# Optimization experiments

Measured on AMD Instinct MI355X. Metric: run time of the kernel, lower is better.

## Reference

```python
import jax, jax.numpy as jnp
import numpy as np

B, K, H, W = 16, 32, 28, 28   # batch, set size, image h, image w
HID, OUT = 64, 64             # hid_dim, out_dim
NOPS = 8                      # permutation-equivariant 3->3 pool/broadcast basis ops


def setup_inputs() -> dict:
    key = jax.random.key(0)
    ks = jax.random.split(key, 8)
    def p(k, shape, fan_in):
        return jax.random.normal(k, shape, jnp.float32) / np.float32(np.sqrt(fan_in))
    return dict(
        x=jax.random.normal(ks[0], (B, K, H, W), jnp.float32),
        conv1_w=p(ks[1], (32, 1, 3, 3), 9),
        conv1_b=jnp.zeros((32,), jnp.float32),
        conv2_w=p(ks[2], (64, 32, 3, 3), 32 * 9),
        conv2_b=jnp.zeros((64,), jnp.float32),
        fc_w=p(ks[3], (HID, 64 * 7 * 7), 64 * 7 * 7),
        fc_b=jnp.zeros((HID,), jnp.float32),
        eq_w=p(ks[4], (HID, OUT, NOPS), HID * NOPS),
        eq_b=jnp.zeros((OUT,), jnp.float32),
        out_w=p(ks[5], (1, OUT), OUT),
        out_b=jnp.zeros((1,), jnp.float32),
    )


def _conv2d(x, w, b):
    y = jax.lax.conv_general_dilated(x, w, (1, 1), 'SAME',
                                     dimension_numbers=('NCHW', 'OIHW', 'NCHW'))
    return y + b[None, :, None, None]


def _maxpool2(x):
    return jax.lax.reduce_window(x, -jnp.inf, jax.lax.max,
                                 (1, 1, 2, 2), (1, 1, 2, 2), 'VALID')


def _forward(x, conv1_w, conv1_b, conv2_w, conv2_b, fc_w, fc_b, eq_w, eq_b, out_w, out_b):
    # --- BasicConvNet embed: (B*K, 1, H, W) -> (B*K, HID) ---
    x1 = x.reshape(B * K, 1, H, W)
    h1 = _maxpool2(jax.nn.relu(_conv2d(x1, conv1_w, conv1_b)))   # (B*K, 32, 14, 14)
    h2 = _maxpool2(jax.nn.relu(_conv2d(h1, conv2_w, conv2_b)))   # (B*K, 64, 7, 7)
    feat = jax.nn.relu(h2.reshape(B * K, -1) @ fc_w.T + fc_b)    # (B*K, HID)
    x4 = feat.reshape(B, K, HID)

    # --- triple outer product: (B, HID, K, K, K), no contracted index ---
    x5 = jnp.einsum('bid,bjd,bkd->bdijk', x4, x4, x4)

    # --- SetEq3to3: 8 equivariant pool/broadcast basis ops, contracted with eq_w[d,e,o].
    # Contract each pooled tensor with its slice of eq_w BEFORE broadcasting (same math,
    # avoids materializing 8 full (B,d,K,K,K) op tensors). ---
    m_i  = x5.mean(2)           # (B, d, j, k)
    m_j  = x5.mean(3)           # (B, d, i, k)
    m_k  = x5.mean(4)           # (B, d, i, j)
    m_ij = m_i.mean(2)          # (B, d, k)
    m_ik = m_i.mean(3)          # (B, d, j)
    m_jk = m_j.mean(3)          # (B, d, i)
    m_all = m_ij.mean(2)        # (B, d)

    x6 = (jnp.einsum('bdijk,de->beijk', x5, eq_w[:, :, 0])
          + jnp.einsum('bdjk,de->bejk', m_i, eq_w[:, :, 1])[:, :, None, :, :]
          + jnp.einsum('bdik,de->beik', m_j, eq_w[:, :, 2])[:, :, :, None, :]
          + jnp.einsum('bdij,de->beij', m_k, eq_w[:, :, 3])[:, :, :, :, None]
          + jnp.einsum('bdk,de->bek', m_ij, eq_w[:, :, 4])[:, :, None, None, :]
          + jnp.einsum('bdj,de->bej', m_ik, eq_w[:, :, 5])[:, :, None, :, None]
          + jnp.einsum('bdi,de->bei', m_jk, eq_w[:, :, 6])[:, :, :, None, None]
          + jnp.einsum('bd,de->be', m_all, eq_w[:, :, 7])[:, :, None, None, None]
          + eq_b[None, :, None, None, None])          # (B, OUT, K, K, K)

    # permute to channels-last, relu, pool over (i,j,k), relu, final linear
    x7 = jax.nn.relu(x6.transpose(0, 2, 3, 4, 1))     # (B, K, K, K, OUT)
    x8 = x7.mean(axis=(1, 2, 3))                      # (B, OUT)
    x9 = jax.nn.relu(x8)
    # dropout_prob = 0 -> identity
    return x9 @ out_w.T + out_b                       # (B, 1)


def reference(x, conv1_w, conv1_b, conv2_w, conv2_b, fc_w, fc_b, eq_w, eq_b, out_w, out_b):
    return _forward(x, conv1_w, conv1_b, conv2_w, conv2_b, fc_w, fc_b,
                    eq_w, eq_b, out_w, out_b)
```

## Files before the change

kernel.cpp:

```cpp
#include <hip/hip_runtime.h>
#include <hip/hip_bf16.h>


typedef __attribute__((ext_vector_type(8))) short short8;
typedef __attribute__((ext_vector_type(4))) float f32x4;

__device__ __forceinline__ f32x4 mfma_bf16(short8 a, short8 b, f32x4 c) {
  return __builtin_amdgcn_mfma_f32_16x16x32_bf16(a, b, c, 0, 0, 0);
}

__device__ __forceinline__ unsigned short f2bs(float f) {
  unsigned int u = __float_as_uint(f);
  unsigned int r = u + 0x7fffu + ((u >> 16) & 1u);
  return (unsigned short)(r >> 16);
}
__device__ __forceinline__ unsigned int pk2(float x, float y) {
  union { __hip_bfloat162 h; unsigned int u; } cv;
  cv.h = __float22bfloat162_rn(make_float2(x, y));
  return cv.u;
}
__device__ __forceinline__ void ub8(const short* p, float* f) {
  uint4 u = *(const uint4*)p;
  f[0] = __uint_as_float(u.x << 16); f[1] = __uint_as_float(u.x & 0xffff0000u);
  f[2] = __uint_as_float(u.y << 16); f[3] = __uint_as_float(u.y & 0xffff0000u);
  f[4] = __uint_as_float(u.z << 16); f[5] = __uint_as_float(u.z & 0xffff0000u);
  f[6] = __uint_as_float(u.w << 16); f[7] = __uint_as_float(u.w & 0xffff0000u);
}

__global__ __launch_bounds__(256, 2) void k12_conv(const float* __restrict__ x,
    const float* __restrict__ w1, const float* __restrict__ b1,
    const float* __restrict__ w2, const float* __restrict__ b2,
    short* __restrict__ h2b,
    const float* __restrict__ eqw, float* __restrict__ W7t, short* __restrict__ Wtb,
    const float* __restrict__ fcw, short* __restrict__ fcwb) {
  const int n = blockIdx.x, t = threadIdx.x;
  if (n >= 512) {
    if (n < 520) {
      const int m = n - 512;
      for (int idx = t; idx < 4096; idx += 256) {
        int e = idx >> 6, d = idx & 63;
        float v = eqw[d*512 + e*8 + m];
        if (m == 7) W7t[idx] = v;
        else        Wtb[m*4096 + idx] = (short)f2bs(v);
      }
    } else {
      int base = (n - 520)*12544 + t;
      for (int q = 0; q < 49; ++q) {
        int idx = base + q*256;
        fcwb[idx] = (short)f2bs(fcw[idx]);
      }
    }
    return;
  }
  __shared__ float si[30*30];
  __shared__ float sw[32*9];
  __shared__ float sb[32];
  __shared__ __align__(16) short inT[16*18*40];
  const int wv = t >> 6, l = t & 63, quad = l >> 4, col = l & 15;

  const int c_out = wv*16 + col;
  float w72[72];
  {
    const float4* src = (const float4*)(w2 + c_out*288 + quad*72);
#pragma unroll
    for (int q = 0; q < 18; ++q) {
      float4 v = src[q];
      w72[q*4+0] = v.x; w72[q*4+1] = v.y; w72[q*4+2] = v.z; w72[q*4+3] = v.w;
    }
  }
  union SU { short8 v; unsigned int u[4]; };
  short8 Bq[9];
#pragma unroll
  for (int dd = 0; dd < 9; ++dd) {
    SU b;
#pragma unroll
    for (int q = 0; q < 4; ++q)
      b.u[q] = pk2(w72[(2*q)*9 + dd], w72[(2*q+1)*9 + dd]);
    Bq[dd] = b.v;
  }
  const float bb2 = b2[c_out];

  for (int idx = t; idx < 900; idx += 256) si[idx] = 0.f;
  {
    unsigned int* zp = (unsigned int*)inT;
    for (int idx = t; idx < 5760; idx += 256) zp[idx] = 0u;
  }
  for (int idx = t; idx < 288; idx += 256) sw[idx] = w1[idx];
  if (t < 32) sb[t] = b1[t];
  __syncthreads();
  for (int idx = t; idx < 784; idx += 256) {
    int y = idx / 28, xx = idx - y*28;
    si[(y+1)*30 + xx + 1] = x[n*784 + idx];
  }
  __syncthreads();

  {
    const int cg = t & 7;
    float wreg[4][9], breg[4];
#pragma unroll
    for (int cc = 0; cc < 4; ++cc) {
      breg[cc] = sb[cg*4 + cc];
#pragma unroll
      for (int q = 0; q < 9; ++q) wreg[cc][q] = sw[(cg*4 + cc)*9 + q];
    }
    for (int idx = t; idx < 1568; idx += 256) {
      int pos = idx >> 3;
      int py = pos / 14, px = pos - py*14;
      float pt[4][4];
#pragma unroll
      for (int r = 0; r < 4; ++r)
#pragma unroll
        for (int q = 0; q < 4; ++q)
          pt[r][q] = si[(2*py + r)*30 + 2*px + q];
      float res[4];
#pragma unroll
      for (int cc = 0; cc < 4; ++cc) {
        float best = 0.f;
#pragma unroll
        for (int a = 0; a < 2; ++a)
#pragma unroll
          for (int b3 = 0; b3 < 2; ++b3) {
            float v = breg[cc]
              + wreg[cc][0]*pt[a+0][b3+0] + wreg[cc][1]*pt[a+0][b3+1] + wreg[cc][2]*pt[a+0][b3+2]
              + wreg[cc][3]*pt[a+1][b3+0] + wreg[cc][4]*pt[a+1][b3+1] + wreg[cc][5]*pt[a+1][b3+2]
              + wreg[cc][6]*pt[a+2][b3+0] + wreg[cc][7]*pt[a+2][b3+1] + wreg[cc][8]*pt[a+2][b3+2];
            best = fmaxf(best, v);
          }
        res[cc] = best;
      }
      uint2 pkd;
      pkd.x = pk2(res[0], res[1]);
      pkd.y = pk2(res[2], res[3]);
      *(uint2*)&inT[(py+1)*720 + (px+1)*40 + cg*4] = pkd;
    }
  }
  __syncthreads();

  for (int p = 0; p < 7; ++p) {
    short8 Ar[4][3];
#pragma unroll
    for (int rr = 0; rr < 4; ++rr)
#pragma unroll
      for (int dx = 0; dx < 3; ++dx)
        Ar[rr][dx] = *(const short8*)&inT[(2*p + rr)*720 + (col + dx)*40 + quad*8];
    f32x4 a0 = {0.f,0.f,0.f,0.f}, a1 = {0.f,0.f,0.f,0.f};
#pragma unroll
    for (int dy = 0; dy < 3; ++dy)
#pragma unroll
      for (int dx = 0; dx < 3; ++dx) {
        a0 = mfma_bf16(Ar[dy][dx],     Bq[dy*3 + dx], a0);
        a1 = mfma_bf16(Ar[dy + 1][dx], Bq[dy*3 + dx], a1);
      }
#pragma unroll
    for (int a = 0; a < 2; ++a) {
      int px = quad*2 + a;
      if (px < 7) {
        float m0 = fmaxf(fmaxf(a0[2*a], a0[2*a + 1]), fmaxf(a1[2*a], a1[2*a + 1]));
        h2b[n*3136 + c_out*49 + p*7 + px] = (short)f2bs(fmaxf(m0 + bb2, 0.f));
      }
    }
  }
}

__global__ __launch_bounds__(256) void k3_mfma(const short* __restrict__ h2b,
    const short* __restrict__ fcwb, float* __restrict__ part) {
  const int blk = blockIdx.x, kp = blockIdx.y, t = threadIdx.x;
  const int w = t >> 6, l = t & 63, quad = l >> 4, col = l & 15;
  const int mt = w & 1, nh = w >> 1;
  const int img = blk*32 + mt*16 + col;
  const short* Ap = h2b + img*3136 + kp*224 + quad*8;
  const short* B0 = fcwb + (nh*32 + col)*3136 + kp*224 + quad*8;
  const short* B1 = fcwb + (nh*32 + 16 + col)*3136 + kp*224 + quad*8;
  f32x4 acc0 = {0.f,0.f,0.f,0.f}, acc1 = {0.f,0.f,0.f,0.f};
#pragma unroll
  for (int q = 0; q < 7; ++q) {
    short8 A  = *(const short8*)(Ap + q*32);
    short8 b0 = *(const short8*)(B0 + q*32);
    short8 b1 = *(const short8*)(B1 + q*32);
    acc0 = mfma_bf16(A, b0, acc0);
    acc1 = mfma_bf16(A, b1, acc1);
  }
  const int e0 = nh*32 + col, e1 = e0 + 16;
  const int base = blk*32 + mt*16 + quad*4;
  float* dst = part + kp*32768;
#pragma unroll
  for (int r = 0; r < 4; ++r) {
    dst[(base + r)*64 + e0] = acc0[r];
    dst[(base + r)*64 + e1] = acc1[r];
  }
}

__global__ __launch_bounds__(256) void k4_prep(const float* __restrict__ part,
    const float* __restrict__ fb, const float* __restrict__ W7t,
    const float* __restrict__ eqb, float* __restrict__ feat,
    float* __restrict__ s, float* __restrict__ t7c) {
  __shared__ __align__(16) float sf[2048];
  __shared__ float ss[64];
  const int b = blockIdx.x, t = threadIdx.x;
  for (int v4 = t; v4 < 512; v4 += 256) {
    float4 a = {0.f, 0.f, 0.f, 0.f};
#pragma unroll
    for (int kp = 0; kp < 14; ++kp) {
      float4 p = *(const float4*)&part[kp*32768 + b*2048 + v4*4];
      a.x += p.x; a.y += p.y; a.z += p.z; a.w += p.w;
    }
    float4 fbv = *(const float4*)&fb[(v4*4) & 63];
    float4 r;
    r.x = fmaxf(a.x + fbv.x, 0.f);
    r.y = fmaxf(a.y + fbv.y, 0.f);
    r.z = fmaxf(a.z + fbv.z, 0.f);
    r.w = fmaxf(a.w + fbv.w, 0.f);
    *(float4*)&sf[v4*4] = r;
    *(float4*)&feat[b*2048 + v4*4] = r;
  }
  __syncthreads();
  if (t < 64) {
    float a = 0.f;
    for (int i = 0; i < 32; ++i) a += sf[i*64 + t];
    a *= (1.f/32.f);
    s[b*64 + t] = a;
    ss[t] = a;
  }
  __syncthreads();
  if (t < 64) {
    const float* W7 = W7t + t*64;
    float t7 = 0.f;
    for (int d = 0; d < 64; ++d) {
      float sv = ss[d];
      t7 += sv*sv*sv * W7[d];
    }
    t7c[b*64 + t] = t7 + eqb[t];
  }
}

__global__ __launch_bounds__(256, 2) void k5_mfma(const float* __restrict__ feat,
    const float* __restrict__ s_, const short* __restrict__ Wtb,
    const float* __restrict__ t7c, float* __restrict__ x8p) {
  __shared__ __align__(16) float Fm[32*68];
  __shared__ __align__(16) float FI[64];
  __shared__ __align__(16) float SV[64];
  __shared__ __align__(16) float C0[64];
  __shared__ float C0P[128];
  __shared__ float KCf[32*68];
  __shared__ float JCf[32*68];
  __shared__ float RED[256];
  __shared__ __align__(16) short Fb[32*72];
  __shared__ __align__(16) short QPb[64*72];
  __shared__ __align__(16) short G2b[64*72];
  __shared__ __align__(16) short G3b[64*72];

  const int i = blockIdx.x, b = blockIdx.y, t = threadIdx.x;
  const int w = t >> 6, l = t & 63, quad = l >> 4, col = l & 15;

  for (int idx = t; idx < 2048; idx += 256) {
    int r = idx >> 6, d = idx & 63;
    float v = feat[b*2048 + idx];
    Fm[r*68 + d] = v;
    Fb[r*72 + d] = (short)f2bs(v);
  }
  if (t < 64) { FI[t] = feat[b*2048 + i*64 + t]; SV[t] = s_[b*64 + t]; }
  __syncthreads();

  {
    const int e = t >> 2, dbase = (t & 3) * 16;
#pragma unroll
    for (int h = 0; h < 2; ++h) {
      int off = dbase + h*8;
      float w0[8], w1[8], w2[8], w3[8], w4[8], w5[8];
      ub8(&Wtb[0*4096 + e*64 + off], w0);
      ub8(&Wtb[1*4096 + e*64 + off], w1);
      ub8(&Wtb[2*4096 + e*64 + off], w2);
      ub8(&Wtb[3*4096 + e*64 + off], w3);
      ub8(&Wtb[4*4096 + e*64 + off], w4);
      ub8(&Wtb[5*4096 + e*64 + off], w5);
      uint4 qv, g2v, g3v;
      unsigned int* qp = &qv.x;
      unsigned int* g2p = &g2v.x;
      unsigned int* g3p = &g3v.x;
#pragma unroll
      for (int j = 0; j < 4; ++j) {
        float fi0 = FI[off + 2*j],     fi1 = FI[off + 2*j + 1];
        float s0  = SV[off + 2*j],     s1  = SV[off + 2*j + 1];
        float q0 = fi0*w0[2*j]   + s0*w1[2*j];
        float q1 = fi1*w0[2*j+1] + s1*w1[2*j+1];
        float a0 = s0*(fi0*w2[2*j]   + s0*w4[2*j]);
        float a1 = s1*(fi1*w2[2*j+1] + s1*w4[2*j+1]);
        float c0 = s0*(fi0*w3[2*j]   + s0*w5[2*j]);
        float c1 = s1*(fi1*w3[2*j+1] + s1*w5[2*j+1]);
        qp[j]  = pk2(q0, q1);
        g2p[j] = pk2(a0, a1);
        g3p[j] = pk2(c0, c1);
      }
      *(uint4*)&QPb[e*72 + off] = qv;
      *(uint4*)&G2b[e*72 + off] = g2v;
      *(uint4*)&G3b[e*72 + off] = g3v;
    }
  }
  if (t < 128) {
    int e = t & 63, dh = t >> 6;
    const short* W6 = Wtb + 6*4096 + e*64 + dh*32;
    float a = 0.f;
#pragma unroll
    for (int g = 0; g < 4; ++g) {
      float wf[8];
      ub8(&W6[g*8], wf);
#pragma unroll
      for (int dd = 0; dd < 8; ++dd) {
        int d = dh*32 + g*8 + dd;
        float sd = SV[d];
        a += sd*sd*FI[d]*wf[dd];
      }
    }
    C0P[dh*64 + e] = a;
  }
  __syncthreads();

  if (w < 2) {
    const short* G = w ? G3b : G2b;
    float* DST = w ? JCf : KCf;
    short8 Bf[4][2];
#pragma unroll
    for (int n = 0; n < 4; ++n)
#pragma unroll
      for (int s2 = 0; s2 < 2; ++s2)
        Bf[n][s2] = *(const short8*)&G[(n*16 + col)*72 + s2*32 + quad*8];
#pragma unroll
    for (int m = 0; m < 2; ++m) {
      short8 A0 = *(const short8*)&Fb[(m*16 + col)*72 + quad*8];
      short8 A1 = *(const short8*)&Fb[(m*16 + col)*72 + 32 + quad*8];
#pragma unroll
      for (int n = 0; n < 4; ++n) {
        f32x4 z = {0.f, 0.f, 0.f, 0.f};
        f32x4 ac = mfma_bf16(A1, Bf[n][1], mfma_bf16(A0, Bf[n][0], z));
#pragma unroll
        for (int r = 0; r < 4; ++r)
          DST[(m*16 + quad*4 + r)*68 + n*16 + col] = ac[r];
      }
    }
  } else if (w == 2) {
    C0[l] = C0P[l] + C0P[64 + l] + t7c[b*64 + l];
  }
  __syncthreads();

  float c0v[4];
#pragma unroll
  for (int n = 0; n < 4; ++n) c0v[n] = C0[n*16 + col];
  float jcq[8][4];
#pragma unroll
  for (int jj = 0; jj < 8; ++jj)
#pragma unroll
    for (int n = 0; n < 4; ++n)
      jcq[jj][n] = JCf[(w*8 + jj)*68 + n*16 + col] + c0v[n];
  float kcv[2][4][4];
#pragma unroll
  for (int kb2 = 0; kb2 < 2; ++kb2)
#pragma unroll
    for (int r = 0; r < 4; ++r)
#pragma unroll
      for (int n = 0; n < 4; ++n)
        kcv[kb2][r][n] = KCf[(kb2*16 + quad*4 + r)*68 + n*16 + col];
  short8 Bq[4][2];
#pragma unroll
  for (int n = 0; n < 4; ++n)
#pragma unroll
    for (int s2 = 0; s2 < 2; ++s2)
      Bq[n][s2] = *(const short8*)&QPb[(n*16 + col)*72 + s2*32 + quad*8];

  float4 fkv[2][4];
#pragma unroll
  for (int kb2 = 0; kb2 < 2; ++kb2) {
    const float* fk = &Fm[(kb2*16 + col)*68 + quad*8];
    fkv[kb2][0] = *(const float4*)(fk);
    fkv[kb2][1] = *(const float4*)(fk + 4);
    fkv[kb2][2] = *(const float4*)(fk + 32);
    fkv[kb2][3] = *(const float4*)(fk + 36);
  }

  float sum[4] = {0.f, 0.f, 0.f, 0.f};
  union SU { short8 v; unsigned int u[4]; };

#pragma unroll
  for (int jj = 0; jj < 8; ++jj) {
    const float* fj = &Fm[(w*8 + jj)*68 + quad*8];
    float4 j0 = *(const float4*)(fj);
    float4 j1 = *(const float4*)(fj + 4);
    float4 j2 = *(const float4*)(fj + 32);
    float4 j3 = *(const float4*)(fj + 36);
#pragma unroll
    for (int kb2 = 0; kb2 < 2; ++kb2) {
      float4 k0 = fkv[kb2][0], k1 = fkv[kb2][1];
      float4 k2v = fkv[kb2][2], k3v = fkv[kb2][3];
      SU A0, A1;
      A0.u[0] = pk2(j0.x*k0.x, j0.y*k0.y);
      A0.u[1] = pk2(j0.z*k0.z, j0.w*k0.w);
      A0.u[2] = pk2(j1.x*k1.x, j1.y*k1.y);
      A0.u[3] = pk2(j1.z*k1.z, j1.w*k1.w);
      A1.u[0] = pk2(j2.x*k2v.x, j2.y*k2v.y);
      A1.u[1] = pk2(j2.z*k2v.z, j2.w*k2v.w);
      A1.u[2] = pk2(j3.x*k3v.x, j3.y*k3v.y);
      A1.u[3] = pk2(j3.z*k3v.z, j3.w*k3v.w);
      f32x4 ac[4];
#pragma unroll
      for (int n = 0; n < 4; ++n) {
        f32x4 z = {0.f, 0.f, 0.f, 0.f};
        ac[n] = mfma_bf16(A1.v, Bq[n][1], mfma_bf16(A0.v, Bq[n][0], z));
      }
#pragma unroll
      for (int n = 0; n < 4; ++n)
#pragma unroll
        for (int r = 0; r < 4; ++r) {
          float v = ac[n][r] + kcv[kb2][r][n] + jcq[jj][n];
          sum[n] += fmaxf(v, 0.f);
        }
    }
  }

#pragma unroll
  for (int n = 0; n < 4; ++n) {
    float v = sum[n];
    v += __shfl_xor(v, 16, 64);
    v += __shfl_xor(v, 32, 64);
    if (l < 16) RED[w*64 + n*16 + l] = v;
  }
  __syncthreads();
  if (t < 64) {
    float tot = RED[t] + RED[64 + t] + RED[128 + t] + RED[192 + t];
    x8p[(b*32 + i)*64 + t] = tot;
  }
}

__global__ __launch_bounds__(64) void k6_out(const float* __restrict__ x8p,
    const float* __restrict__ ow, const float* __restrict__ ob,
    float* __restrict__ out) {
  const int bb = blockIdx.x, t = threadIdx.x;
  float a = 0.f;
#pragma unroll
  for (int i = 0; i < 32; ++i) a += x8p[(bb*32 + i)*64 + t];
  float v = fmaxf(a * (1.f/32768.f), 0.f) * ow[t];
#pragma unroll
  for (int off = 32; off > 0; off >>= 1) v += __shfl_down(v, off, 64);
  if (t == 0) out[bb] = v + ob[0];
}

extern "C" void kernel_launch(void* const* d_in, const int* in_sizes, int n_in,
                              void* d_out, int out_size, void* d_ws, size_t ws_size,
                              hipStream_t stream) {
  const float* x   = (const float*)d_in[0];
  const float* c1w = (const float*)d_in[1];
  const float* c1b = (const float*)d_in[2];
  const float* c2w = (const float*)d_in[3];
  const float* c2b = (const float*)d_in[4];
  const float* fcw = (const float*)d_in[5];
  const float* fcb = (const float*)d_in[6];
  const float* eqw = (const float*)d_in[7];
  const float* eqb = (const float*)d_in[8];
  const float* ow  = (const float*)d_in[9];
  const float* ob  = (const float*)d_in[10];
  float* out = (float*)d_out;

  short* h2b  = (short*)d_ws;
  float* feat = (float*)(h2b + 512*3136);
  float* s    = feat + 32768;
  float* t7c  = s + 1024;
  float* x8p  = t7c + 1024;
  float* W7t  = x8p + 32768;
  short* Wtb  = (short*)(W7t + 4096);
  short* fcwb = Wtb + 7*4096;
  float* part = (float*)(fcwb + 200704);

  hipLaunchKernelGGL(k12_conv, dim3(536), dim3(256), 0, stream,
                     x, c1w, c1b, c2w, c2b, h2b, eqw, W7t, Wtb, fcw, fcwb);
  hipLaunchKernelGGL(k3_mfma,  dim3(16, 14), dim3(256), 0, stream, h2b, fcwb, part);
  hipLaunchKernelGGL(k4_prep,  dim3(16),  dim3(256), 0, stream,
                     part, fcb, W7t, eqb, feat, s, t7c);
  hipLaunchKernelGGL(k5_mfma,  dim3(32, 16), dim3(256), 0, stream, feat, s, Wtb, t7c, x8p);
  hipLaunchKernelGGL(k6_out,   dim3(16),  dim3(64),  0, stream, x8p, ow, ob, out);
}
```

Measured before the change: 122.9 us.

## Fuse FC layer into conv kernel and move set-mean prep into equivariant kernel

Weight conversion moves into a separate small prep kernel, which also pre-packs conv2 weights into bf16 MFMA fragment order so each conv block loads them directly. The conv kernel now keeps pooled conv2 output in shared memory and computes the FC layer per image with a scalar dot product, removing the bf16 h2 round-trip, the split-K partial buffer, and the k3/k4 launches. The set mean and cubic term are recomputed inside each equivariant block. In exchange, every conv block streams the full bf16 FC weight matrix, the FC uses scalar FMAs instead of MFMA, the shared-memory footprint grows, and the prep kernel now runs serially before the conv.

```diff
diff --git a/kernel.cpp b/kernel.cpp
--- a/kernel.cpp
+++ b/kernel.cpp
@@ -27,56 +27,53 @@
   f[6] = __uint_as_float(u.w << 16); f[7] = __uint_as_float(u.w & 0xffff0000u);
 }
 
-__global__ __launch_bounds__(256, 2) void k12_conv(const float* __restrict__ x,
+__global__ __launch_bounds__(256) void k0_prep(const float* __restrict__ eqw,
+    const float* __restrict__ w2, const float* __restrict__ fcw,
+    float* __restrict__ W7t, short* __restrict__ Wtb,
+    short* __restrict__ w2p, short* __restrict__ fcwb) {
+  const int b = blockIdx.x, t = threadIdx.x;
+  if (b < 8) {
+    const int m = b;
+    for (int idx = t; idx < 4096; idx += 256) {
+      int e = idx >> 6, d = idx & 63;
+      float v = eqw[d*512 + e*8 + m];
+      if (m == 7) W7t[idx] = v;
+      else        Wtb[m*4096 + idx] = (short)f2bs(v);
+    }
+  } else if (b == 8) {
+    for (int idx = t; idx < 18432; idx += 256) {
+      int s2 = idx & 7, c = (idx >> 3) & 63, quad = (idx >> 9) & 3, dd = idx >> 11;
+      w2p[idx] = (short)f2bs(w2[c*288 + (quad*8 + s2)*9 + dd]);
+    }
+  } else {
+    int base = (b - 9)*12544 + t;
+    for (int q = 0; q < 49; ++q) {
+      int idx = base + q*256;
+      fcwb[idx] = (short)f2bs(fcw[idx]);
+    }
+  }
+}
+
+__global__ __launch_bounds__(256, 2) void kA_conv(const float* __restrict__ x,
     const float* __restrict__ w1, const float* __restrict__ b1,
-    const float* __restrict__ w2, const float* __restrict__ b2,
-    short* __restrict__ h2b,
-    const float* __restrict__ eqw, float* __restrict__ W7t, short* __restrict__ Wtb,
-    const float* __restrict__ fcw, short* __restrict__ fcwb) {
+    const short* __restrict__ w2p, const float* __restrict__ b2,
+    const short* __restrict__ fcwb, const float* __restrict__ fcb,
+    float* __restrict__ feat) {
   const int n = blockIdx.x, t = threadIdx.x;
-  if (n >= 512) {
-    if (n < 520) {
-      const int m = n - 512;
-      for (int idx = t; idx < 4096; idx += 256) {
-        int e = idx >> 6, d = idx & 63;
-        float v = eqw[d*512 + e*8 + m];
-        if (m == 7) W7t[idx] = v;
-        else        Wtb[m*4096 + idx] = (short)f2bs(v);
-      }
-    } else {
-      int base = (n - 520)*12544 + t;
-      for (int q = 0; q < 49; ++q) {
-        int idx = base + q*256;
-        fcwb[idx] = (short)f2bs(fcw[idx]);
-      }
-    }
-    return;
-  }
   __shared__ float si[30*30];
   __shared__ float sw[32*9];
   __shared__ float sb[32];
   __shared__ __align__(16) short inT[16*18*40];
+  __shared__ __align__(16) float h2f[3136];
+  __shared__ float sf4[256];
   const int wv = t >> 6, l = t & 63, quad = l >> 4, col = l & 15;
 
   const int c_out = wv*16 + col;
-  float w72[72];
+  short8 Bq[9];
   {
-    const float4* src = (const float4*)(w2 + c_out*288 + quad*72);
-#pragma unroll
-    for (int q = 0; q < 18; ++q) {
-      float4 v = src[q];
-      w72[q*4+0] = v.x; w72[q*4+1] = v.y; w72[q*4+2] = v.z; w72[q*4+3] = v.w;
-    }
-  }
-  union SU { short8 v; unsigned int u[4]; };
-  short8 Bq[9];
-#pragma unroll
-  for (int dd = 0; dd < 9; ++dd) {
-    SU b;
-#pragma unroll
-    for (int q = 0; q < 4; ++q)
-      b.u[q] = pk2(w72[(2*q)*9 + dd], w72[(2*q+1)*9 + dd]);
-    Bq[dd] = b.v;
+    const short8* wp = (const short8*)w2p + quad*64 + c_out;
+#pragma unroll
+    for (int dd = 0; dd < 9; ++dd) Bq[dd] = wp[dd*256];
   }
   const float bb2 = b2[c_out];
 
@@ -156,89 +153,41 @@
       int px = quad*2 + a;
       if (px < 7) {
         float m0 = fmaxf(fmaxf(a0[2*a], a0[2*a + 1]), fmaxf(a1[2*a], a1[2*a + 1]));
-        h2b[n*3136 + c_out*49 + p*7 + px] = (short)f2bs(fmaxf(m0 + bb2, 0.f));
-      }
-    }
-  }
-}
-
-__global__ __launch_bounds__(256) void k3_mfma(const short* __restrict__ h2b,
-    const short* __restrict__ fcwb, float* __restrict__ part) {
-  const int blk = blockIdx.x, kp = blockIdx.y, t = threadIdx.x;
-  const int w = t >> 6, l = t & 63, quad = l >> 4, col = l & 15;
-  const int mt = w & 1, nh = w >> 1;
-  const int img = blk*32 + mt*16 + col;
-  const short* Ap = h2b + img*3136 + kp*224 + quad*8;
-  const short* B0 = fcwb + (nh*32 + col)*3136 + kp*224 + quad*8;
-  const short* B1 = fcwb + (nh*32 + 16 + col)*3136 + kp*224 + quad*8;
-  f32x4 acc0 = {0.f,0.f,0.f,0.f}, acc1 = {0.f,0.f,0.f,0.f};
-#pragma unroll
-  for (int q = 0; q < 7; ++q) {
-    short8 A  = *(const short8*)(Ap + q*32);
-    short8 b0 = *(const short8*)(B0 + q*32);
-    short8 b1 = *(const short8*)(B1 + q*32);
-    acc0 = mfma_bf16(A, b0, acc0);
-    acc1 = mfma_bf16(A, b1, acc1);
-  }
-  const int e0 = nh*32 + col, e1 = e0 + 16;
-  const int base = blk*32 + mt*16 + quad*4;
-  float* dst = part + kp*32768;
-#pragma unroll
-  for (int r = 0; r < 4; ++r) {
-    dst[(base + r)*64 + e0] = acc0[r];
-    dst[(base + r)*64 + e1] = acc1[r];
-  }
-}
-
-__global__ __launch_bounds__(256) void k4_prep(const float* __restrict__ part,
-    const float* __restrict__ fb, const float* __restrict__ W7t,
-    const float* __restrict__ eqb, float* __restrict__ feat,
-    float* __restrict__ s, float* __restrict__ t7c) {
-  __shared__ __align__(16) float sf[2048];
-  __shared__ float ss[64];
-  const int b = blockIdx.x, t = threadIdx.x;
-  for (int v4 = t; v4 < 512; v4 += 256) {
-    float4 a = {0.f, 0.f, 0.f, 0.f};
-#pragma unroll
-    for (int kp = 0; kp < 14; ++kp) {
-      float4 p = *(const float4*)&part[kp*32768 + b*2048 + v4*4];
-      a.x += p.x; a.y += p.y; a.z += p.z; a.w += p.w;
-    }
-    float4 fbv = *(const float4*)&fb[(v4*4) & 63];
-    float4 r;
-    r.x = fmaxf(a.x + fbv.x, 0.f);
-    r.y = fmaxf(a.y + fbv.y, 0.f);
-    r.z = fmaxf(a.z + fbv.z, 0.f);
-    r.w = fmaxf(a.w + fbv.w, 0.f);
-    *(float4*)&sf[v4*4] = r;
-    *(float4*)&feat[b*2048 + v4*4] = r;
+        h2f[c_out*49 + p*7 + px] = fmaxf(m0 + bb2, 0.f);
+      }
+    }
+  }
+  {
+    const short* Wrow = fcwb + l*3136 + wv*784;
+    const float* Hrow = h2f + wv*784;
+    float a0 = 0.f, a1 = 0.f, a2 = 0.f, a3 = 0.f;
+#pragma unroll 7
+    for (int j = 0; j < 98; ++j) {
+      float wf[8]; ub8(&Wrow[j*8], wf);
+      float4 hx = *(const float4*)&Hrow[j*8];
+      float4 hy = *(const float4*)&Hrow[j*8 + 4];
+      a0 += wf[0]*hx.x + wf[4]*hy.x;
+      a1 += wf[1]*hx.y + wf[5]*hy.y;
+      a2 += wf[2]*hx.z + wf[6]*hy.z;
+      a3 += wf[3]*hx.w + wf[7]*hy.w;
+    }
+    sf4[wv*64 + l] = (a0 + a1) + (a2 + a3);
   }
   __syncthreads();
   if (t < 64) {
-    float a = 0.f;
-    for (int i = 0; i < 32; ++i) a += sf[i*64 + t];
-    a *= (1.f/32.f);
-    s[b*64 + t] = a;
-    ss[t] = a;
-  }
-  __syncthreads();
-  if (t < 64) {
-    const float* W7 = W7t + t*64;
-    float t7 = 0.f;
-    for (int d = 0; d < 64; ++d) {
-      float sv = ss[d];
-      t7 += sv*sv*sv * W7[d];
-    }
-    t7c[b*64 + t] = t7 + eqb[t];
+    float v = sf4[t] + sf4[64 + t] + sf4[128 + t] + sf4[192 + t] + fcb[t];
+    feat[n*64 + t] = fmaxf(v, 0.f);
   }
 }
 
 __global__ __launch_bounds__(256, 2) void k5_mfma(const float* __restrict__ feat,
-    const float* __restrict__ s_, const short* __restrict__ Wtb,
-    const float* __restrict__ t7c, float* __restrict__ x8p) {
+    const short* __restrict__ Wtb, const float* __restrict__ W7t,
+    const float* __restrict__ eqb, float* __restrict__ x8p) {
   __shared__ __align__(16) float Fm[32*68];
   __shared__ __align__(16) float FI[64];
   __shared__ __align__(16) float SV[64];
+  __shared__ __align__(16) float SC[64];
+  __shared__ __align__(16) float TC[64];
   __shared__ __align__(16) float C0[64];
   __shared__ float C0P[128];
   __shared__ float KCf[32*68];
@@ -258,21 +207,42 @@
     Fm[r*68 + d] = v;
     Fb[r*72 + d] = (short)f2bs(v);
   }
-  if (t < 64) { FI[t] = feat[b*2048 + i*64 + t]; SV[t] = s_[b*64 + t]; }
-  __syncthreads();
+  if (t < 64) FI[t] = feat[b*2048 + i*64 + t];
+  __syncthreads();
+
+  if (t < 64) {
+    float a = 0.f;
+#pragma unroll
+    for (int r = 0; r < 32; ++r) a += Fm[r*68 + t];
+    a *= (1.f/32.f);
+    SV[t] = a;
+    SC[t] = a*a*a;
+  }
+  __syncthreads();
+
+  if (t < 64) {
+    const float* W7 = W7t + t*64;
+    float acc = 0.f;
+#pragma unroll
+    for (int d = 0; d < 64; d += 4) {
+      float4 w4 = *(const float4*)&W7[d];
+      acc += SC[d]*w4.x + SC[d+1]*w4.y + SC[d+2]*w4.z + SC[d+3]*w4.w;
+    }
+    TC[t] = acc + eqb[t];
+  }
 
   {
     const int e = t >> 2, dbase = (t & 3) * 16;
 #pragma unroll
     for (int h = 0; h < 2; ++h) {
       int off = dbase + h*8;
-      float w0[8], w1[8], w2[8], w3[8], w4[8], w5[8];
+      float w0[8], w1r[8], w2r[8], w3r[8], w4r[8], w5r[8];
       ub8(&Wtb[0*4096 + e*64 + off], w0);
-      ub8(&Wtb[1*4096 + e*64 + off], w1);
-      ub8(&Wtb[2*4096 + e*64 + off], w2);
-      ub8(&Wtb[3*4096 + e*64 + off], w3);
-      ub8(&Wtb[4*4096 + e*64 + off], w4);
-      ub8(&Wtb[5*4096 + e*64 + off], w5);
+      ub8(&Wtb[1*4096 + e*64 + off], w1r);
+      ub8(&Wtb[2*4096 + e*64 + off], w2r);
+      ub8(&Wtb[3*4096 + e*64 + off], w3r);
+      ub8(&Wtb[4*4096 + e*64 + off], w4r);
+      ub8(&Wtb[5*4096 + e*64 + off], w5r);
       uint4 qv, g2v, g3v;
       unsigned int* qp = &qv.x;
       unsigned int* g2p = &g2v.x;
@@ -281,12 +251,12 @@
       for (int j = 0; j < 4; ++j) {
         float fi0 = FI[off + 2*j],     fi1 = FI[off + 2*j + 1];
         float s0  = SV[off + 2*j],     s1  = SV[off + 2*j + 1];
-        float q0 = fi0*w0[2*j]   + s0*w1[2*j];
-        float q1 = fi1*w0[2*j+1] + s1*w1[2*j+1];
-        float a0 = s0*(fi0*w2[2*j]   + s0*w4[2*j]);
-        float a1 = s1*(fi1*w2[2*j+1] + s1*w4[2*j+1]);
-        float c0 = s0*(fi0*w3[2*j]   + s0*w5[2*j]);
-        float c1 = s1*(fi1*w3[2*j+1] + s1*w5[2*j+1]);
+        float q0 = fi0*w0[2*j]   + s0*w1r[2*j];
+        float q1 = fi1*w0[2*j+1] + s1*w1r[2*j+1];
+        float a0 = s0*(fi0*w2r[2*j]   + s0*w4r[2*j]);
+        float a1 = s1*(fi1*w2r[2*j+1] + s1*w4r[2*j+1]);
+        float c0 = s0*(fi0*w3r[2*j]   + s0*w5r[2*j]);
+        float c1 = s1*(fi1*w3r[2*j+1] + s1*w5r[2*j+1]);
         qp[j]  = pk2(q0, q1);
         g2p[j] = pk2(a0, a1);
         g3p[j] = pk2(c0, c1);
@@ -338,7 +308,7 @@
       }
     }
   } else if (w == 2) {
-    C0[l] = C0P[l] + C0P[64 + l] + t7c[b*64 + l];
+    C0[l] = C0P[l] + C0P[64 + l] + TC[l];
   }
   __syncthreads();
 
@@ -458,21 +428,19 @@
   const float* ob  = (const float*)d_in[10];
   float* out = (float*)d_out;
 
-  short* h2b  = (short*)d_ws;
-  float* feat = (float*)(h2b + 512*3136);
-  float* s    = feat + 32768;
-  float* t7c  = s + 1024;
-  float* x8p  = t7c + 1024;
+  float* feat = (float*)d_ws;
+  float* x8p  = feat + 32768;
   float* W7t  = x8p + 32768;
   short* Wtb  = (short*)(W7t + 4096);
-  short* fcwb = Wtb + 7*4096;
-  float* part = (float*)(fcwb + 200704);
-
-  hipLaunchKernelGGL(k12_conv, dim3(536), dim3(256), 0, stream,
-                     x, c1w, c1b, c2w, c2b, h2b, eqw, W7t, Wtb, fcw, fcwb);
-  hipLaunchKernelGGL(k3_mfma,  dim3(16, 14), dim3(256), 0, stream, h2b, fcwb, part);
-  hipLaunchKernelGGL(k4_prep,  dim3(16),  dim3(256), 0, stream,
-                     part, fcb, W7t, eqb, feat, s, t7c);
-  hipLaunchKernelGGL(k5_mfma,  dim3(32, 16), dim3(256), 0, stream, feat, s, Wtb, t7c, x8p);
-  hipLaunchKernelGGL(k6_out,   dim3(16),  dim3(64),  0, stream, x8p, ow, ob, out);
-}
+  short* w2p  = Wtb + 28672;
+  short* fcwb = w2p + 18432;
+  (void)in_sizes; (void)n_in; (void)out_size; (void)ws_size;
+
+  hipLaunchKernelGGL(k0_prep, dim3(25), dim3(256), 0, stream,
+                     eqw, c2w, fcw, W7t, Wtb, w2p, fcwb);
+  hipLaunchKernelGGL(kA_conv, dim3(512), dim3(256), 0, stream,
+                     x, c1w, c1b, w2p, c2b, fcwb, fcb, feat);
+  hipLaunchKernelGGL(k5_mfma, dim3(32, 16), dim3(256), 0, stream,
+                     feat, Wtb, W7t, eqb, x8p);
+  hipLaunchKernelGGL(k6_out,  dim3(16),  dim3(64),  0, stream, x8p, ow, ob, out);
+}
```

After: 138.9 us. 1.13x slower.
